# Optimization experiments

Measured on AMD Instinct MI355X. Metric: run time of the kernel, lower is better.

The kernel has to match this reference:

```python
import jax, jax.numpy as jnp
import numpy as np

B, N_CAM, J = 8, 5, 15        # batch, cameras, joints
H, W = 128, 240               # heatmap h, w  (HEATMAP_SIZE = [240, 128] = [w, h])
VX, VY, VZ = 80, 80, 20       # voxels_per_axis
NBINS = VX * VY * VZ          # 128000


def setup_inputs() -> dict:
    key = jax.random.key(0)
    k1, k2 = jax.random.split(key)
    heatmaps = jax.random.uniform(k1, (B, N_CAM, J, H, W), dtype=jnp.float32)
    # cached projected sampling grid, clamped to [-1.1, 1.1] as in project_grid
    sample_grid = jax.random.uniform(k2, (N_CAM, NBINS, 2), dtype=jnp.float32,
                                     minval=-1.1, maxval=1.1)
    return {"heatmaps": heatmaps, "sample_grid": sample_grid}


def _grid_sample_bilinear(hm, grid):
    """F.grid_sample(mode='bilinear', padding_mode='zeros', align_corners=True).

    hm:   [B, n, J, H, W]
    grid: [n, nbins, 2]  normalized (x, y) in roughly [-1.1, 1.1]
    returns [B, n, J, nbins]
    """
    Bv, n, Jv, Hv, Wv = hm.shape
    nb = grid.shape[1]
    gx, gy = grid[..., 0], grid[..., 1]
    # align_corners=True mapping from [-1, 1] to pixel coords
    ix = (gx + 1.0) * 0.5 * (Wv - 1)
    iy = (gy + 1.0) * 0.5 * (Hv - 1)
    x0 = jnp.floor(ix)
    y0 = jnp.floor(iy)
    x1 = x0 + 1.0
    y1 = y0 + 1.0
    wx1 = ix - x0
    wx0 = 1.0 - wx1
    wy1 = iy - y0
    wy0 = 1.0 - wy1

    hmf = hm.reshape(Bv, n, Jv, Hv * Wv)

    def gather(yi, xi):
        # zeros padding: out-of-range corners contribute 0
        valid = ((xi >= 0) & (xi <= Wv - 1) & (yi >= 0) & (yi <= Hv - 1))
        xc = jnp.clip(xi, 0, Wv - 1).astype(jnp.int32)
        yc = jnp.clip(yi, 0, Hv - 1).astype(jnp.int32)
        idx = yc * Wv + xc                                   # [n, nb]
        idxb = jnp.broadcast_to(idx[None, :, None, :], (Bv, n, Jv, nb))
        vals = jnp.take_along_axis(hmf, idxb, axis=3)        # [B, n, J, nb]
        return vals * valid[None, :, None, :].astype(hm.dtype)

    out = (gather(y0, x0) * (wy0 * wx0)[None, :, None, :]
           + gather(y0, x1) * (wy0 * wx1)[None, :, None, :]
           + gather(y1, x0) * (wy1 * wx0)[None, :, None, :]
           + gather(y1, x1) * (wy1 * wx1)[None, :, None, :])
    return out


def reference(heatmaps, sample_grid):
    sampled = _grid_sample_bilinear(heatmaps, sample_grid)   # [B, n, J, nbins]
    cubes = jnp.clip(jnp.mean(sampled, axis=1), 0.0, 1.0)    # mean over cameras
    return cubes.reshape(heatmaps.shape[0], heatmaps.shape[2], VX, VY, VZ)
```

## Files before the change

### kernel.cpp

```cpp
#include <hip/hip_runtime.h>
#include <hip/hip_fp16.h>

#define B_     8
#define NCAM   5
#define J_     15
#define H_     128
#define W_     240
#define NB     128000
#define HW_    (H_ * W_)
#define OV_ROWS (H_ - 1)
#define OV_DW   (OV_ROWS * W_)
#define SMEM_BYTES (OV_DW * 4)
#define OV_G4   (OV_DW / 4)
#define TPB    1024
#define NCHUNK 4
#define BPB    (NB / NCHUNK)
#define ITEMS  32
#define NBJ    (B_ * J_)
#define NBLK   (NBJ * NCHUNK)

typedef __fp16 fp16x2 __attribute__((ext_vector_type(2)));

__device__ __forceinline__ unsigned int pkrtz(float lo, float hi) {
    fp16x2 h = __builtin_amdgcn_cvt_pkrtz(lo, hi);
    return __builtin_bit_cast(unsigned int, h);
}

__device__ __forceinline__ void bilinear_rec(float gx, float gy,
                                             unsigned int& addr,
                                             unsigned int& w0pk,
                                             unsigned int& w1pk) {
    const float ix = (gx + 1.0f) * (0.5f * (W_ - 1));
    const float iy = (gy + 1.0f) * (0.5f * (H_ - 1));
    const float x0f = floorf(ix);
    const float y0f = floorf(iy);
    const float wx1 = ix - x0f, wx0 = 1.0f - wx1;
    const float wy1 = iy - y0f, wy0 = 1.0f - wy1;
    const int x0 = (int)x0f;
    const int y0 = (int)y0f;
    const int xc = min(max(x0, 0), W_ - 2);
    const int yc = min(max(y0, 0), H_ - 2);
    const float vx0 = (x0 >= 0  && x0 <= W_ - 1) ? wx0 : 0.0f;
    const float vx1 = (x0 >= -1 && x0 <= W_ - 2) ? wx1 : 0.0f;
    const float vy0 = (y0 >= 0  && y0 <= H_ - 1) ? wy0 : 0.0f;
    const float vy1 = (y0 >= -1 && y0 <= H_ - 2) ? wy1 : 0.0f;
    const bool xhi = (x0 == W_ - 1);
    const bool xlo = (x0 == -1);
    const bool yhi = (y0 == H_ - 1);
    const bool ylo = (y0 == -1);
    const float a0 = (xhi ? 0.0f : vx0) + (xlo ? vx1 : 0.0f);
    const float a1 = (xhi ? vx0 : 0.0f) + (xlo ? 0.0f : vx1);
    const float b0 = (yhi ? 0.0f : vy0) + (ylo ? vy1 : 0.0f);
    const float b1 = (yhi ? vy0 : 0.0f) + (ylo ? 0.0f : vy1);
    addr = (unsigned int)(yc * W_ + xc);
    w0pk = pkrtz(0.2f * (a0 * b0), 0.2f * (a0 * b1));
    w1pk = pkrtz(0.2f * (a1 * b0), 0.2f * (a1 * b1));
}

__global__ __launch_bounds__(256) void weights_kernel(
    const float* __restrict__ sgrid,
    unsigned short* __restrict__ addr16,
    uint2* __restrict__ wpk)
{
    const int i = blockIdx.x * 256 + threadIdx.x;
    if (i >= NCAM * NB) return;
    const float2 g = ((const float2*)sgrid)[i];
    unsigned int a, w0, w1;
    bilinear_rec(g.x, g.y, a, w0, w1);
    addr16[i] = (unsigned short)a;
    wpk[i] = make_uint2(w0, w1);
}

__device__ __forceinline__ void stage_overlap(const float* __restrict__ img,
                                              unsigned int* s_img, int tid) {
    const float4* __restrict__ src4 = (const float4*)img;
    uint4* dst = (uint4*)s_img;
    for (int gi = tid; gi < OV_G4; gi += TPB) {
        const int y  = gi / 60;
        const int xg = gi - y * 60;
        const float4 t = src4[y * 60 + xg];
        const float4 b = src4[y * 60 + 60 + xg];
        uint4 d;
        d.x = pkrtz(t.x, b.x);
        d.y = pkrtz(t.y, b.y);
        d.z = pkrtz(t.z, b.z);
        d.w = pkrtz(t.w, b.w);
        dst[gi] = d;
    }
}

__device__ __forceinline__ float sample_ov(const unsigned int* s_img,
                                           unsigned int a16,
                                           unsigned int w0, unsigned int w1) {
    const unsigned int* base = s_img + a16;
    const unsigned int d0 = base[0];
    const unsigned int d1 = base[1];
    __half2 p = __hmul2(__builtin_bit_cast(__half2, d0),
                        __builtin_bit_cast(__half2, w0));
    p = __hfma2(__builtin_bit_cast(__half2, d1),
                __builtin_bit_cast(__half2, w1), p);
    return __low2float(p) + __high2float(p);
}

__global__ __launch_bounds__(TPB, 4) void project_kernel(
    const float* __restrict__ hm,
    const unsigned short* __restrict__ addr16,
    const uint2* __restrict__ wpk,
    float* __restrict__ out)
{
    extern __shared__ unsigned int s_img[];
    const int tid   = threadIdx.x;
    const int bj    = blockIdx.x % NBJ;
    const int chunk = blockIdx.x / NBJ;
    const int b     = bj / J_;
    const int j     = bj % J_;
    const int bin0  = chunk * BPB;

    float acc[ITEMS];
#pragma unroll
    for (int it = 0; it < ITEMS; ++it) acc[it] = 0.0f;

    for (int n = 0; n < NCAM; ++n) {
        __syncthreads();
        stage_overlap(hm + (((size_t)b * NCAM + n) * J_ + j) * HW_, s_img, tid);
        __syncthreads();
        const unsigned short* __restrict__ ap = addr16 + n * NB + bin0;
        const uint2* __restrict__ wp = wpk + n * NB + bin0;
#pragma unroll
        for (int it = 0; it < ITEMS; ++it) {
            const int r = it * TPB + tid;
            if (r < BPB) {
                acc[it] += sample_ov(s_img, ap[r], wp[r].x, wp[r].y);
            }
        }
    }

    float* __restrict__ o = out + (size_t)bj * NB + bin0;
#pragma unroll
    for (int it = 0; it < ITEMS; ++it) {
        const int r = it * TPB + tid;
        if (r < BPB) o[r] = fminf(fmaxf(acc[it], 0.0f), 1.0f);
    }
}

#define FB_SMEM   (HW_ * 4)
#define FB_NCHUNK 5
#define FB_BPB    (NB / FB_NCHUNK)
#define FB_ITEMS  (FB_BPB / TPB)
__global__ __launch_bounds__(TPB) void project_fallback(
    const float* __restrict__ hm,
    const float* __restrict__ sgrid,
    float* __restrict__ out)
{
    extern __shared__ float s_f32[];
    const int tid   = threadIdx.x;
    const int bj    = blockIdx.x % NBJ;
    const int chunk = blockIdx.x / NBJ;
    const int b     = bj / J_;
    const int j     = bj % J_;
    const int bin0  = chunk * FB_BPB;

    float acc[FB_ITEMS];
#pragma unroll
    for (int it = 0; it < FB_ITEMS; ++it) acc[it] = 0.0f;

    for (int n = 0; n < NCAM; ++n) {
        __syncthreads();
        const float4* __restrict__ src =
            (const float4*)(hm + (((size_t)b * NCAM + n) * J_ + j) * HW_);
        float4* dst = (float4*)s_f32;
        for (int i = tid; i < HW_ / 4; i += TPB) dst[i] = src[i];
        __syncthreads();
        const float2* __restrict__ g2 = (const float2*)sgrid + n * NB + bin0;
#pragma unroll
        for (int it = 0; it < FB_ITEMS; ++it) {
            const float2 g = g2[it * TPB + tid];
            const float ix = (g.x + 1.0f) * (0.5f * (W_ - 1));
            const float iy = (g.y + 1.0f) * (0.5f * (H_ - 1));
            const float x0f = floorf(ix), y0f = floorf(iy);
            const float wx1 = ix - x0f, wx0 = 1.0f - wx1;
            const float wy1 = iy - y0f, wy0 = 1.0f - wy1;
            const int x0 = (int)x0f, y0 = (int)y0f;
            const int xc = min(max(x0, 0), W_ - 2);
            const int yc = min(max(y0, 0), H_ - 2);
            const float vx0 = (x0 >= 0  && x0 <= W_ - 1) ? wx0 : 0.0f;
            const float vx1 = (x0 >= -1 && x0 <= W_ - 2) ? wx1 : 0.0f;
            const float vy0 = (y0 >= 0  && y0 <= H_ - 1) ? wy0 : 0.0f;
            const float vy1 = (y0 >= -1 && y0 <= H_ - 2) ? wy1 : 0.0f;
            const bool xhi = (x0 == W_ - 1), xlo = (x0 == -1);
            const bool yhi = (y0 == H_ - 1), ylo = (y0 == -1);
            const float a0 = (xhi ? 0.0f : vx0) + (xlo ? vx1 : 0.0f);
            const float a1 = (xhi ? vx0 : 0.0f) + (xlo ? 0.0f : vx1);
            const float b0 = (yhi ? 0.0f : vy0) + (ylo ? vy1 : 0.0f);
            const float b1 = (yhi ? vy0 : 0.0f) + (ylo ? 0.0f : vy1);
            const float* r0 = s_f32 + (yc * W_ + xc);
            acc[it] += b0 * (a0 * r0[0] + a1 * r0[1])
                     + b1 * (a0 * r0[W_] + a1 * r0[W_ + 1]);
        }
    }
    float* __restrict__ o = out + (size_t)bj * NB + bin0;
#pragma unroll
    for (int it = 0; it < FB_ITEMS; ++it)
        o[it * TPB + tid] = fminf(fmaxf(acc[it] * 0.2f, 0.0f), 1.0f);
}

extern "C" void kernel_launch(void* const* d_in, const int* in_sizes, int n_in,
                              void* d_out, int out_size, void* d_ws, size_t ws_size,
                              hipStream_t stream) {
    const float* hm = (const float*)d_in[0];
    const float* sg = (const float*)d_in[1];
    float* out = (float*)d_out;

    (void)hipFuncSetAttribute((const void*)project_kernel,
                              hipFuncAttributeMaxDynamicSharedMemorySize, SMEM_BYTES);
    (void)hipFuncSetAttribute((const void*)project_fallback,
                              hipFuncAttributeMaxDynamicSharedMemorySize, FB_SMEM);

    const size_t addr_bytes = (size_t)NCAM * NB * sizeof(unsigned short);
    const size_t wpk_bytes  = (size_t)NCAM * NB * sizeof(uint2);
    if (ws_size >= addr_bytes + wpk_bytes) {
        unsigned short* addr16 = (unsigned short*)d_ws;
        uint2* wpk = (uint2*)((char*)d_ws + addr_bytes);
        weights_kernel<<<(NCAM * NB + 255) / 256, 256, 0, stream>>>(sg, addr16, wpk);
        project_kernel<<<NBLK, TPB, SMEM_BYTES, stream>>>(hm, addr16, wpk, out);
    } else {
        project_fallback<<<NBJ * FB_NCHUNK, TPB, FB_SMEM, stream>>>(hm, sg, out);
    }
}
```

Baseline: 213.3 us.

## Software-pipeline weight loads and LDS reads, use fdot2 for sampling

After: 426.2 us. 2x slower.

```diff
diff --git a/kernel.cpp b/kernel.cpp
--- a/kernel.cpp
+++ b/kernel.cpp
@@ -18,12 +18,25 @@
 #define ITEMS  32
 #define NBJ    (B_ * J_)
 #define NBLK   (NBJ * NCHUNK)
+#define GRP    4
+#define NGRP   (ITEMS / GRP)
 
 typedef __fp16 fp16x2 __attribute__((ext_vector_type(2)));
 
 __device__ __forceinline__ unsigned int pkrtz(float lo, float hi) {
     fp16x2 h = __builtin_amdgcn_cvt_pkrtz(lo, hi);
     return __builtin_bit_cast(unsigned int, h);
+}
+
+__device__ __forceinline__ float fdot2(unsigned int d, unsigned int w, float c) {
+#if __has_builtin(__builtin_amdgcn_fdot2)
+    return __builtin_amdgcn_fdot2(__builtin_bit_cast(fp16x2, d),
+                                  __builtin_bit_cast(fp16x2, w), c, false);
+#else
+    __half2 p = __hmul2(__builtin_bit_cast(__half2, d),
+                        __builtin_bit_cast(__half2, w));
+    return c + __low2float(p) + __high2float(p);
+#endif
 }
 
 __device__ __forceinline__ void bilinear_rec(float gx, float gy,
@@ -89,18 +102,53 @@
     }
 }
 
-__device__ __forceinline__ float sample_ov(const unsigned int* s_img,
-                                           unsigned int a16,
-                                           unsigned int w0, unsigned int w1) {
-    const unsigned int* base = s_img + a16;
-    const unsigned int d0 = base[0];
-    const unsigned int d1 = base[1];
-    __half2 p = __hmul2(__builtin_bit_cast(__half2, d0),
-                        __builtin_bit_cast(__half2, w0));
-    p = __hfma2(__builtin_bit_cast(__half2, d1),
-                __builtin_bit_cast(__half2, w1), p);
-    return __low2float(p) + __high2float(p);
-}
+struct WRec {
+    unsigned int a[GRP];
+    uint2 w[GRP];
+};
+
+template <int G>
+__device__ __forceinline__ void load_grp(const unsigned short* __restrict__ ap,
+                                         const uint2* __restrict__ wp,
+                                         int tid, bool tail_ok, WRec& W) {
+#pragma unroll
+    for (int u = 0; u < GRP; ++u) {
+        constexpr int it = G * GRP;
+        const int r = (it + u) * TPB + tid;
+        if (it + u < ITEMS - 1 || tail_ok) {
+            W.a[u] = ap[r];
+            W.w[u] = wp[r];
+        } else {
+            W.a[u] = 0;
+            W.w[u] = make_uint2(0u, 0u);
+        }
+    }
+}
+
+__device__ __forceinline__ void read_grp(const unsigned int* s_img, const WRec& W,
+                                         unsigned int* d0, unsigned int* d1) {
+#pragma unroll
+    for (int u = 0; u < GRP; ++u) {
+        const unsigned int* base = s_img + W.a[u];
+        d0[u] = base[0];
+        d1[u] = base[1];
+    }
+}
+
+template <int G>
+__device__ __forceinline__ void fma_grp(const WRec& W, const unsigned int* d0,
+                                        const unsigned int* d1, float* acc) {
+#pragma unroll
+    for (int u = 0; u < GRP; ++u) {
+        const float t = fdot2(d0[u], W.w[u].x, acc[G * GRP + u]);
+        acc[G * GRP + u] = fdot2(d1[u], W.w[u].y, t);
+    }
+}
+
+#define COPY_W(dst, src) do { _Pragma("unroll") \
+    for (int _u = 0; _u < GRP; ++_u) { (dst).a[_u] = (src).a[_u]; (dst).w[_u] = (src).w[_u]; } } while (0)
+#define COPY_D(dst, src) do { _Pragma("unroll") \
+    for (int _u = 0; _u < GRP; ++_u) (dst)[_u] = (src)[_u]; } while (0)
 
 __global__ __launch_bounds__(TPB, 4) void project_kernel(
     const float* __restrict__ hm,
@@ -115,6 +163,7 @@
     const int b     = bj / J_;
     const int j     = bj % J_;
     const int bin0  = chunk * BPB;
+    const bool tail_ok = (tid < BPB - (ITEMS - 1) * TPB);
 
     float acc[ITEMS];
 #pragma unroll
@@ -126,12 +175,39 @@
         __syncthreads();
         const unsigned short* __restrict__ ap = addr16 + n * NB + bin0;
         const uint2* __restrict__ wp = wpk + n * NB + bin0;
-#pragma unroll
-        for (int it = 0; it < ITEMS; ++it) {
-            const int r = it * TPB + tid;
-            if (r < BPB) {
-                acc[it] += sample_ov(s_img, ap[r], wp[r].x, wp[r].y);
+
+        WRec Wa, Wb, Wc;
+        unsigned int d0a[GRP], d1a[GRP], d0b[GRP], d1b[GRP];
+        load_grp<0>(ap, wp, tid, tail_ok, Wa);
+        load_grp<1>(ap, wp, tid, tail_ok, Wb);
+        read_grp(s_img, Wa, d0a, d1a);
+#pragma unroll
+        for (int g = 0; g < NGRP; ++g) {
+            if (g + 2 < NGRP) {
+                switch (g) {
+                    case 0: load_grp<2>(ap, wp, tid, tail_ok, Wc); break;
+                    case 1: load_grp<3>(ap, wp, tid, tail_ok, Wc); break;
+                    case 2: load_grp<4>(ap, wp, tid, tail_ok, Wc); break;
+                    case 3: load_grp<5>(ap, wp, tid, tail_ok, Wc); break;
+                    case 4: load_grp<6>(ap, wp, tid, tail_ok, Wc); break;
+                    case 5: load_grp<7>(ap, wp, tid, tail_ok, Wc); break;
+                }
             }
+            if (g + 1 < NGRP) read_grp(s_img, Wb, d0b, d1b);
+            switch (g) {
+                case 0: fma_grp<0>(Wa, d0a, d1a, acc); break;
+                case 1: fma_grp<1>(Wa, d0a, d1a, acc); break;
+                case 2: fma_grp<2>(Wa, d0a, d1a, acc); break;
+                case 3: fma_grp<3>(Wa, d0a, d1a, acc); break;
+                case 4: fma_grp<4>(Wa, d0a, d1a, acc); break;
+                case 5: fma_grp<5>(Wa, d0a, d1a, acc); break;
+                case 6: fma_grp<6>(Wa, d0a, d1a, acc); break;
+                case 7: fma_grp<7>(Wa, d0a, d1a, acc); break;
+            }
+            COPY_W(Wa, Wb);
+            COPY_W(Wb, Wc);
+            COPY_D(d0a, d0b);
+            COPY_D(d1a, d1b);
         }
     }
 
```

## Software-pipeline gather loop with prefetch, sched barriers, and fdot2 accumulation

Applied to the files above, without the earlier changes.

Result: slower. 425.7 us (+99.5%).

```diff
diff --git a/kernel.cpp b/kernel.cpp
--- a/kernel.cpp
+++ b/kernel.cpp
@@ -24,6 +24,17 @@
 __device__ __forceinline__ unsigned int pkrtz(float lo, float hi) {
     fp16x2 h = __builtin_amdgcn_cvt_pkrtz(lo, hi);
     return __builtin_bit_cast(unsigned int, h);
+}
+
+__device__ __forceinline__ float fdot2(unsigned int d, unsigned int w, float c) {
+#if __has_builtin(__builtin_amdgcn_fdot2)
+    return __builtin_amdgcn_fdot2(__builtin_bit_cast(fp16x2, d),
+                                  __builtin_bit_cast(fp16x2, w), c, false);
+#else
+    __half2 p = __hmul2(__builtin_bit_cast(__half2, d),
+                        __builtin_bit_cast(__half2, w));
+    return c + __low2float(p) + __high2float(p);
+#endif
 }
 
 __device__ __forceinline__ void bilinear_rec(float gx, float gy,
@@ -89,18 +100,29 @@
     }
 }
 
-__device__ __forceinline__ float sample_ov(const unsigned int* s_img,
-                                           unsigned int a16,
-                                           unsigned int w0, unsigned int w1) {
-    const unsigned int* base = s_img + a16;
-    const unsigned int d0 = base[0];
-    const unsigned int d1 = base[1];
-    __half2 p = __hmul2(__builtin_bit_cast(__half2, d0),
-                        __builtin_bit_cast(__half2, w0));
-    p = __hfma2(__builtin_bit_cast(__half2, d1),
-                __builtin_bit_cast(__half2, w1), p);
-    return __low2float(p) + __high2float(p);
-}
+#define LOADI(G, U) \
+    const unsigned int a##U##_##G = ap[((G)*4 + (U)) * TPB + tid]; \
+    const uint2        w##U##_##G = wp[((G)*4 + (U)) * TPB + tid];
+#define LOADB(G) LOADI(G, 0) LOADI(G, 1) LOADI(G, 2) LOADI(G, 3)
+#define LOADB7 \
+    LOADI(7, 0) LOADI(7, 1) LOADI(7, 2) \
+    const unsigned int a3_7 = tail_ok ? (unsigned int)ap[31 * TPB + tid] : 0u; \
+    const uint2        w3_7 = tail_ok ? wp[31 * TPB + tid] : make_uint2(0u, 0u);
+
+#define LDSI(G, U) \
+    const unsigned int p##U##_##G = s_img[a##U##_##G]; \
+    const unsigned int q##U##_##G = s_img[a##U##_##G + 1u];
+#define LDSB(G) LDSI(G, 0) LDSI(G, 1) LDSI(G, 2) LDSI(G, 3)
+
+#define DOTI(G, U) \
+    acc[(G)*4 + (U)] = fdot2(q##U##_##G, w##U##_##G.y, \
+                       fdot2(p##U##_##G, w##U##_##G.x, acc[(G)*4 + (U)]));
+#define DOTB(G) DOTI(G, 0) DOTI(G, 1) DOTI(G, 2) DOTI(G, 3)
+
+#define SBAR __builtin_amdgcn_sched_barrier(0)
+
+#define ZI(IT)  acc[IT] = 0.0f;
+#define OUTI(IT) o[(IT) * TPB + tid] = fminf(fmaxf(acc[IT], 0.0f), 1.0f);
 
 __global__ __launch_bounds__(TPB, 4) void project_kernel(
     const float* __restrict__ hm,
@@ -108,39 +130,45 @@
     const uint2* __restrict__ wpk,
     float* __restrict__ out)
 {
-    extern __shared__ unsigned int s_img[];
+    __shared__ unsigned int s_img[OV_DW];
     const int tid   = threadIdx.x;
     const int bj    = blockIdx.x % NBJ;
     const int chunk = blockIdx.x / NBJ;
     const int b     = bj / J_;
     const int j     = bj % J_;
     const int bin0  = chunk * BPB;
+    const bool tail_ok = (tid < BPB - (ITEMS - 1) * TPB);
 
     float acc[ITEMS];
-#pragma unroll
-    for (int it = 0; it < ITEMS; ++it) acc[it] = 0.0f;
+    ZI(0) ZI(1) ZI(2) ZI(3) ZI(4) ZI(5) ZI(6) ZI(7)
+    ZI(8) ZI(9) ZI(10) ZI(11) ZI(12) ZI(13) ZI(14) ZI(15)
+    ZI(16) ZI(17) ZI(18) ZI(19) ZI(20) ZI(21) ZI(22) ZI(23)
+    ZI(24) ZI(25) ZI(26) ZI(27) ZI(28) ZI(29) ZI(30) ZI(31)
 
     for (int n = 0; n < NCAM; ++n) {
-        __syncthreads();
-        stage_overlap(hm + (((size_t)b * NCAM + n) * J_ + j) * HW_, s_img, tid);
-        __syncthreads();
         const unsigned short* __restrict__ ap = addr16 + n * NB + bin0;
         const uint2* __restrict__ wp = wpk + n * NB + bin0;
-#pragma unroll
-        for (int it = 0; it < ITEMS; ++it) {
-            const int r = it * TPB + tid;
-            if (r < BPB) {
-                acc[it] += sample_ov(s_img, ap[r], wp[r].x, wp[r].y);
-            }
-        }
+        LOADB(0) LOADB(1)
+        __syncthreads();
+        stage_overlap(hm + (((size_t)b * NCAM + n) * J_ + j) * HW_, s_img, tid);
+        __syncthreads();
+        LDSB(0) LOADB(2)          SBAR;
+        LDSB(1) LOADB(3) DOTB(0)  SBAR;
+        LDSB(2) LOADB(4) DOTB(1)  SBAR;
+        LDSB(3) LOADB(5) DOTB(2)  SBAR;
+        LDSB(4) LOADB(6) DOTB(3)  SBAR;
+        LDSB(5) LOADB7   DOTB(4)  SBAR;
+        LDSB(6)          DOTB(5)  SBAR;
+        LDSB(7)          DOTB(6)  SBAR;
+                         DOTB(7)
     }
 
     float* __restrict__ o = out + (size_t)bj * NB + bin0;
-#pragma unroll
-    for (int it = 0; it < ITEMS; ++it) {
-        const int r = it * TPB + tid;
-        if (r < BPB) o[r] = fminf(fmaxf(acc[it], 0.0f), 1.0f);
-    }
+    OUTI(0) OUTI(1) OUTI(2) OUTI(3) OUTI(4) OUTI(5) OUTI(6) OUTI(7)
+    OUTI(8) OUTI(9) OUTI(10) OUTI(11) OUTI(12) OUTI(13) OUTI(14) OUTI(15)
+    OUTI(16) OUTI(17) OUTI(18) OUTI(19) OUTI(20) OUTI(21) OUTI(22) OUTI(23)
+    OUTI(24) OUTI(25) OUTI(26) OUTI(27) OUTI(28) OUTI(29) OUTI(30)
+    if (tail_ok) { OUTI(31) }
 }
 
 #define FB_SMEM   (HW_ * 4)
@@ -211,8 +239,6 @@
     const float* sg = (const float*)d_in[1];
     float* out = (float*)d_out;
 
-    (void)hipFuncSetAttribute((const void*)project_kernel,
-                              hipFuncAttributeMaxDynamicSharedMemorySize, SMEM_BYTES);
     (void)hipFuncSetAttribute((const void*)project_fallback,
                               hipFuncAttributeMaxDynamicSharedMemorySize, FB_SMEM);
 
@@ -222,7 +248,7 @@
         unsigned short* addr16 = (unsigned short*)d_ws;
         uint2* wpk = (uint2*)((char*)d_ws + addr_bytes);
         weights_kernel<<<(NCAM * NB + 255) / 256, 256, 0, stream>>>(sg, addr16, wpk);
-        project_kernel<<<NBLK, TPB, SMEM_BYTES, stream>>>(hm, addr16, wpk, out);
+        project_kernel<<<NBLK, TPB, 0, stream>>>(hm, addr16, wpk, out);
     } else {
         project_fallback<<<NBJ * FB_NCHUNK, TPB, FB_SMEM, stream>>>(hm, sg, out);
     }
```
